# Kernel optimization log

Measured on AMD Instinct MI355X. Metric: run time of the kernel, lower is better.

The kernel has to match this reference:

```python
import jax, jax.numpy as jnp
import numpy as np

NUM_HEADS = 8
HEAD_DIM = 16


def setup_inputs() -> dict:
    key = jax.random.key(0)
    ks = jax.random.split(key, 9)
    B, S, E, H = 2, 4096, 16, 128
    sc_in = 1.0 / np.sqrt(E)
    sc_h = 1.0 / np.sqrt(H)
    return {
        "x": jax.random.normal(ks[0], (B, S, E), dtype=jnp.float32),
        "wq": jax.random.normal(ks[1], (H, E), dtype=jnp.float32) * sc_in,
        "bq": jax.random.normal(ks[2], (H,), dtype=jnp.float32) * 0.02,
        "wk": jax.random.normal(ks[3], (H, E), dtype=jnp.float32) * sc_in,
        "bk": jax.random.normal(ks[4], (H,), dtype=jnp.float32) * 0.02,
        "wv": jax.random.normal(ks[5], (H, E), dtype=jnp.float32) * sc_in,
        "bv": jax.random.normal(ks[6], (H,), dtype=jnp.float32) * 0.02,
        "wo": jax.random.normal(ks[7], (E, H), dtype=jnp.float32) * sc_h,
        "bo": jax.random.normal(ks[8], (E,), dtype=jnp.float32) * 0.02,
    }


def reference(x, wq, bq, wk, bk, wv, bv, wo, bo):
    B, S, E = x.shape
    H = wq.shape[0]
    nh, hd = NUM_HEADS, HEAD_DIM
    # QKV projections (torch Linear: y = x @ W.T + b)
    q = x @ wq.T + bq  # [B,S,H]
    k = x @ wk.T + bk
    v = x @ wv.T + bv
    # split heads -> [B,nh,S,hd]
    q = q.reshape(B, S, nh, hd).transpose(0, 2, 1, 3)
    k = k.reshape(B, S, nh, hd).transpose(0, 2, 1, 3)
    v = v.reshape(B, S, nh, hd).transpose(0, 2, 1, 3)
    # flex_attention with block_mask=None == full SDPA, scale = 1/sqrt(head_dim)
    scale = 1.0 / np.sqrt(hd)
    scores = jnp.einsum("bhqd,bhkd->bhqk", q, k) * scale  # [B,nh,S,S]
    attn = jax.nn.softmax(scores, axis=-1)
    out = jnp.einsum("bhqk,bhkd->bhqd", attn, v)  # [B,nh,S,hd]
    out = out.transpose(0, 2, 1, 3).reshape(B, S, H)
    return out @ wo.T + bo
```

## Files before the change

kernel.cpp:

```cpp
#include <hip/hip_runtime.h>
#include <hip/hip_bf16.h>
#include <math.h>

#define NH 8
#define HD 16
#define EE 16
#define HH 128
#define NCH 4
#define QR 32

typedef __attribute__((ext_vector_type(8)))  short short8;
typedef __attribute__((ext_vector_type(16))) float f32x16;
typedef __attribute__((ext_vector_type(4)))  float f32x4;

#define EXP2F(x) __builtin_amdgcn_exp2f(x)

__global__ __launch_bounds__(256) void qkv_fused(
        const float* __restrict__ x,
        const float* __restrict__ wq, const float* __restrict__ bq,
        const float* __restrict__ wk, const float* __restrict__ bk,
        const float* __restrict__ wv, const float* __restrict__ bv,
        __hip_bfloat16* __restrict__ Qb, __hip_bfloat16* __restrict__ Kb,
        __hip_bfloat16* __restrict__ Vt, int S) {
    int row0 = blockIdx.x * QR;
    int b = row0 / S, s0 = row0 - b * S;
    int tid = threadIdx.x;

    __shared__ __align__(16) float xs[QR][EE];
    __shared__ __align__(16) short qsb[QR][136];
    __shared__ __align__(16) short ksb[QR][136];
    __shared__ __align__(16) short vsb[QR][136];

    ((float*)xs)[tid]       = x[(size_t)row0 * EE + tid];
    ((float*)xs)[tid + 256] = x[(size_t)row0 * EE + tid + 256];
    __syncthreads();

    int h = tid & 127, sub = tid >> 7;
    float wqr[16], wkr[16], wvr[16];
    const float4* wq4 = (const float4*)(wq + h * EE);
    const float4* wk4 = (const float4*)(wk + h * EE);
    const float4* wv4 = (const float4*)(wv + h * EE);
#pragma unroll
    for (int j = 0; j < 4; ++j) {
        float4 a = wq4[j]; wqr[4*j]=a.x; wqr[4*j+1]=a.y; wqr[4*j+2]=a.z; wqr[4*j+3]=a.w;
        float4 c = wk4[j]; wkr[4*j]=c.x; wkr[4*j+1]=c.y; wkr[4*j+2]=c.z; wkr[4*j+3]=c.w;
        float4 d = wv4[j]; wvr[4*j]=d.x; wvr[4*j+1]=d.y; wvr[4*j+2]=d.z; wvr[4*j+3]=d.w;
    }
    float bqv = bq[h], bkv = bk[h], bvv = bv[h];

#pragma unroll
    for (int rr = 0; rr < 16; ++rr) {
        int r = (sub << 4) + rr;
        const float4* xv = (const float4*)xs[r];
        float aq = bqv, ak = bkv, av = bvv;
#pragma unroll
        for (int j = 0; j < 4; ++j) {
            float4 xe = xv[j];
            aq += xe.x*wqr[4*j] + xe.y*wqr[4*j+1] + xe.z*wqr[4*j+2] + xe.w*wqr[4*j+3];
            ak += xe.x*wkr[4*j] + xe.y*wkr[4*j+1] + xe.z*wkr[4*j+2] + xe.w*wkr[4*j+3];
            av += xe.x*wvr[4*j] + xe.y*wvr[4*j+1] + xe.z*wvr[4*j+2] + xe.w*wvr[4*j+3];
        }
        __hip_bfloat16 qb = __float2bfloat16(aq * 0.36067376022f);
        __hip_bfloat16 kb = __float2bfloat16(ak);
        __hip_bfloat16 vb = __float2bfloat16(av);
        qsb[r][h] = *reinterpret_cast<short*>(&qb);
        ksb[r][h] = *reinterpret_cast<short*>(&kb);
        vsb[r][h] = *reinterpret_cast<short*>(&vb);
    }
    __syncthreads();

    {
        int r = tid & 31, head = tid >> 5;
        short8 a = *(const short8*)&qsb[r][head * 16];
        short8 c = *(const short8*)&qsb[r][head * 16 + 8];
        short* dst = (short*)Qb + ((size_t)(b * NH + head) * S + s0 + r) * HD;
        *(short8*)dst = a;
        *(short8*)(dst + 8) = c;
        a = *(const short8*)&ksb[r][head * 16];
        c = *(const short8*)&ksb[r][head * 16 + 8];
        dst = (short*)Kb + ((size_t)(b * NH + head) * S + s0 + r) * HD;
        *(short8*)dst = a;
        *(short8*)(dst + 8) = c;
    }
    {
        int hd_idx = tid >> 1;
        int head2 = hd_idx >> 4, d2 = hd_idx & 15;
        int si0 = (tid & 1) * 16;
        short8 w0, w1;
#pragma unroll
        for (int j = 0; j < 8; ++j) w0[j] = vsb[si0 + j][hd_idx];
#pragma unroll
        for (int j = 0; j < 8; ++j) w1[j] = vsb[si0 + 8 + j][hd_idx];
        short* dst = (short*)Vt + ((size_t)(b * NH + head2) * HD + d2) * S + s0 + si0;
        *(short8*)dst = w0;
        *(short8*)(dst + 8) = w1;
    }
}

__global__ __launch_bounds__(256, 8) void attn(const __hip_bfloat16* __restrict__ Qb,
                                               const __hip_bfloat16* __restrict__ Kb,
                                               const __hip_bfloat16* __restrict__ Vtb,
                                               float* __restrict__ A,
                                               int S, int BH) {
    int bh = blockIdx.y;
    int q0 = blockIdx.x * 32;
    int cb = threadIdx.x >> 6;
    int lane = threadIdx.x & 63;
    int ql = lane & 31, half = lane >> 5;
    int l15 = lane & 15, l4 = lane >> 4;
    int CS = S / NCH;
    int kbeg = cb * CS;

    __shared__ __align__(16) union {
        short pt[NCH][32 * 40];
        struct { float o[NCH][32][16]; float l[NCH][32]; } red;
    } sm;
    short* pt = sm.pt[cb];

    const short* qptr = (const short*)Qb + ((size_t)bh * S + q0) * HD;
    const short* kf_ptr = (const short*)Kb + ((size_t)bh * S + kbeg + ql) * HD + 8 * half;
    const short* vf_ptr = (const short*)Vtb + ((size_t)bh * HD + l15) * S + kbeg + 8 * l4;

    short8 qf = *(const short8*)(qptr + ql * HD + 8 * half);

    f32x16 zc;
#pragma unroll
    for (int i = 0; i < 16; ++i) zc[i] = 0.f;

    float l = 0.f;
    f32x4 o0, o1;
#pragma unroll
    for (int i = 0; i < 4; ++i) { o0[i] = 0.f; o1[i] = 0.f; }

    for (int it = 0; it < CS / 32; ++it) {
        short8 kf = *(const short8*)kf_ptr;
        kf_ptr += 32 * HD;
        f32x16 st = __builtin_amdgcn_mfma_f32_32x32x16_bf16(kf, qf, zc, 0, 0, 0);

        float pf[16];
#pragma unroll
        for (int r = 0; r < 16; ++r) pf[r] = EXP2F(st[r]);
        float rs = ((pf[0] + pf[1]) + (pf[2] + pf[3])) + ((pf[4] + pf[5]) + (pf[6] + pf[7]))
                 + ((pf[8] + pf[9]) + (pf[10] + pf[11])) + ((pf[12] + pf[13]) + (pf[14] + pf[15]));
        l += rs;

        union PU { __hip_bfloat162 b2; unsigned u; };
        unsigned pk[8];
#pragma unroll
        for (int i = 0; i < 8; ++i) {
            float2 f2; f2.x = pf[2 * i]; f2.y = pf[2 * i + 1];
            PU pu; pu.b2 = __float22bfloat162_rn(f2);
            pk[i] = pu.u;
        }
#pragma unroll
        for (int i = 0; i < 4; ++i) {
            uint2 w; w.x = pk[2 * i]; w.y = pk[2 * i + 1];
            *(uint2*)&pt[ql * 40 + 8 * i + 4 * half] = w;
        }
        short8 p0 = *(const short8*)&pt[l15 * 40 + 8 * l4];
        short8 p1 = *(const short8*)&pt[(l15 + 16) * 40 + 8 * l4];
        short8 vf = *(const short8*)vf_ptr;
        vf_ptr += 32;

        o0 = __builtin_amdgcn_mfma_f32_16x16x32_bf16(vf, p0, o0, 0, 0, 0);
        o1 = __builtin_amdgcn_mfma_f32_16x16x32_bf16(vf, p1, o1, 0, 0, 0);
    }

    l += __shfl_xor(l, 32);

    __syncthreads();
    {
        float4 r0; r0.x = o0[0]; r0.y = o0[1]; r0.z = o0[2]; r0.w = o0[3];
        float4 r1; r1.x = o1[0]; r1.y = o1[1]; r1.z = o1[2]; r1.w = o1[3];
        *(float4*)&sm.red.o[cb][l15][4 * l4]      = r0;
        *(float4*)&sm.red.o[cb][l15 + 16][4 * l4] = r1;
        if (half == 0) sm.red.l[cb][ql] = l;
    }
    __syncthreads();

    if (threadIdx.x < 128) {
        int q = threadIdx.x >> 2, quad = threadIdx.x & 3;
        float4 acc; acc.x = 0.f; acc.y = 0.f; acc.z = 0.f; acc.w = 0.f;
        float ls = 0.f;
#pragma unroll
        for (int c = 0; c < NCH; ++c) {
            float4 v = *(const float4*)&sm.red.o[c][q][4 * quad];
            acc.x += v.x; acc.y += v.y; acc.z += v.z; acc.w += v.w;
            ls += sm.red.l[c][q];
        }
        float inv = 1.f / ls;
        acc.x *= inv; acc.y *= inv; acc.z *= inv; acc.w *= inv;
        int b = bh >> 3, head = bh & 7;
        *(float4*)&A[((size_t)(b * S + q0 + q)) * HH + head * HD + 4 * quad] = acc;
    }
}

__global__ __launch_bounds__(256) void out_proj(
        const float* __restrict__ A, const float* __restrict__ wo,
        const float* __restrict__ bo, float* __restrict__ out, int rows) {
    __shared__ float As[16][HH + 1];
    __shared__ float ws[EE][HH + 1];
    int r0 = blockIdx.x * 16;
    int tid = threadIdx.x;
#pragma unroll
    for (int i = 0; i < 8; ++i) {
        int idx = tid + i * 256;
        ws[idx >> 7][idx & 127] = wo[idx];
        As[idx >> 7][idx & 127] = A[(size_t)r0 * HH + idx];
    }
    __syncthreads();
    int r = tid >> 4, e = tid & 15;
    float acc = bo[e];
#pragma unroll
    for (int h = 0; h < HH; ++h) acc += As[r][h] * ws[e][h];
    out[(size_t)(r0 + r) * EE + e] = acc;
}

extern "C" void kernel_launch(void* const* d_in, const int* in_sizes, int n_in,
                              void* d_out, int out_size, void* d_ws, size_t ws_size,
                              hipStream_t stream) {
    const float* x  = (const float*)d_in[0];
    const float* wq = (const float*)d_in[1];
    const float* bq = (const float*)d_in[2];
    const float* wk = (const float*)d_in[3];
    const float* bk = (const float*)d_in[4];
    const float* wv = (const float*)d_in[5];
    const float* bv = (const float*)d_in[6];
    const float* wo = (const float*)d_in[7];
    const float* bo = (const float*)d_in[8];
    float* out = (float*)d_out;

    int rows = in_sizes[0] / EE;
    int S = 4096;
    int B = rows / S;
    int BH = B * NH;

    size_t n = (size_t)rows * HH;
    __hip_bfloat16* Qb = (__hip_bfloat16*)d_ws;
    __hip_bfloat16* Kb = Qb + n;
    __hip_bfloat16* Vt = Kb + n;
    float* A = (float*)(Vt + n);

    qkv_fused<<<rows / QR, 256, 0, stream>>>(x, wq, bq, wk, bk, wv, bv, Qb, Kb, Vt, S);
    dim3 g2(S / 32, BH);
    attn<<<g2, 256, 0, stream>>>(Qb, Kb, Vt, A, S, BH);
    out_proj<<<rows / 16, 256, 0, stream>>>(A, wo, bo, out, rows);
}
```

Before: 129.0 us.

## Fuse output projection into attention via per-head atomics; halve QKV tile rows

The output projection now runs in the attention kernel's epilogue. Each head block multiplies its normalized 32x16 output by its 16-column slice of wo, adds bo/NH, and atomically accumulates into the output, which is zeroed with a memset first. This removes the separate out_proj launch and the fp32 intermediate A's write and read. It costs a memset, 8-way atomic contention per output element and a non-deterministic summation order. Separately, the QKV kernel processes 16 rows per block instead of 32, which doubles the block count.

```diff
diff --git a/kernel.cpp b/kernel.cpp
--- a/kernel.cpp
+++ b/kernel.cpp
@@ -7,7 +7,7 @@
 #define EE 16
 #define HH 128
 #define NCH 4
-#define QR 32
+#define QR 16
 
 typedef __attribute__((ext_vector_type(8)))  short short8;
 typedef __attribute__((ext_vector_type(16))) float f32x16;
@@ -31,8 +31,7 @@
     __shared__ __align__(16) short ksb[QR][136];
     __shared__ __align__(16) short vsb[QR][136];
 
-    ((float*)xs)[tid]       = x[(size_t)row0 * EE + tid];
-    ((float*)xs)[tid + 256] = x[(size_t)row0 * EE + tid + 256];
+    ((float*)xs)[tid] = x[(size_t)row0 * EE + tid];
     __syncthreads();
 
     int h = tid & 127, sub = tid >> 7;
@@ -49,8 +48,8 @@
     float bqv = bq[h], bkv = bk[h], bvv = bv[h];
 
 #pragma unroll
-    for (int rr = 0; rr < 16; ++rr) {
-        int r = (sub << 4) + rr;
+    for (int rr = 0; rr < 8; ++rr) {
+        int r = (sub << 3) + rr;
         const float4* xv = (const float4*)xs[r];
         float aq = bqv, ak = bkv, av = bvv;
 #pragma unroll
@@ -70,37 +69,40 @@
     __syncthreads();
 
     {
-        int r = tid & 31, head = tid >> 5;
-        short8 a = *(const short8*)&qsb[r][head * 16];
-        short8 c = *(const short8*)&qsb[r][head * 16 + 8];
-        short* dst = (short*)Qb + ((size_t)(b * NH + head) * S + s0 + r) * HD;
-        *(short8*)dst = a;
-        *(short8*)(dst + 8) = c;
-        a = *(const short8*)&ksb[r][head * 16];
-        c = *(const short8*)&ksb[r][head * 16 + 8];
-        dst = (short*)Kb + ((size_t)(b * NH + head) * S + s0 + r) * HD;
-        *(short8*)dst = a;
-        *(short8*)(dst + 8) = c;
+        int pr = tid & 127;
+        int r = pr & 15, head = pr >> 4;
+        if (tid < 128) {
+            short8 a = *(const short8*)&qsb[r][head * 16];
+            short8 c = *(const short8*)&qsb[r][head * 16 + 8];
+            short* dst = (short*)Qb + ((size_t)(b * NH + head) * S + s0 + r) * HD;
+            *(short8*)dst = a;
+            *(short8*)(dst + 8) = c;
+        } else {
+            short8 a = *(const short8*)&ksb[r][head * 16];
+            short8 c = *(const short8*)&ksb[r][head * 16 + 8];
+            short* dst = (short*)Kb + ((size_t)(b * NH + head) * S + s0 + r) * HD;
+            *(short8*)dst = a;
+            *(short8*)(dst + 8) = c;
+        }
     }
     {
         int hd_idx = tid >> 1;
         int head2 = hd_idx >> 4, d2 = hd_idx & 15;
-        int si0 = (tid & 1) * 16;
-        short8 w0, w1;
+        int si0 = (tid & 1) * 8;
+        short8 w0;
 #pragma unroll
         for (int j = 0; j < 8; ++j) w0[j] = vsb[si0 + j][hd_idx];
-#pragma unroll
-        for (int j = 0; j < 8; ++j) w1[j] = vsb[si0 + 8 + j][hd_idx];
         short* dst = (short*)Vt + ((size_t)(b * NH + head2) * HD + d2) * S + s0 + si0;
         *(short8*)dst = w0;
-        *(short8*)(dst + 8) = w1;
     }
 }
 
 __global__ __launch_bounds__(256, 8) void attn(const __hip_bfloat16* __restrict__ Qb,
                                                const __hip_bfloat16* __restrict__ Kb,
                                                const __hip_bfloat16* __restrict__ Vtb,
-                                               float* __restrict__ A,
+                                               const float* __restrict__ wo,
+                                               const float* __restrict__ bo,
+                                               float* __restrict__ Out,
                                                int S, int BH) {
     int bh = blockIdx.y;
     int q0 = blockIdx.x * 32;
@@ -115,6 +117,7 @@
         short pt[NCH][32 * 40];
         struct { float o[NCH][32][16]; float l[NCH][32]; } red;
     } sm;
+    __shared__ __align__(16) float onorm[32][16];
     short* pt = sm.pt[cb];
 
     const short* qptr = (const short*)Qb + ((size_t)bh * S + q0) * HD;
@@ -190,30 +193,26 @@
         }
         float inv = 1.f / ls;
         acc.x *= inv; acc.y *= inv; acc.z *= inv; acc.w *= inv;
-        int b = bh >> 3, head = bh & 7;
-        *(float4*)&A[((size_t)(b * S + q0 + q)) * HH + head * HD + 4 * quad] = acc;
-    }
-}
-
-__global__ __launch_bounds__(256) void out_proj(
-        const float* __restrict__ A, const float* __restrict__ wo,
-        const float* __restrict__ bo, float* __restrict__ out, int rows) {
-    __shared__ float As[16][HH + 1];
-    __shared__ float ws[EE][HH + 1];
-    int r0 = blockIdx.x * 16;
-    int tid = threadIdx.x;
-#pragma unroll
-    for (int i = 0; i < 8; ++i) {
-        int idx = tid + i * 256;
-        ws[idx >> 7][idx & 127] = wo[idx];
-        As[idx >> 7][idx & 127] = A[(size_t)r0 * HH + idx];
-    }
-    __syncthreads();
-    int r = tid >> 4, e = tid & 15;
-    float acc = bo[e];
-#pragma unroll
-    for (int h = 0; h < HH; ++h) acc += As[r][h] * ws[e][h];
-    out[(size_t)(r0 + r) * EE + e] = acc;
+        *(float4*)&onorm[q][4 * quad] = acc;
+    }
+    __syncthreads();
+
+    int b = bh >> 3, head = bh & 7;
+#pragma unroll
+    for (int i = 0; i < 2; ++i) {
+        int p = threadIdx.x + 256 * i;
+        int q = p >> 4, e = p & 15;
+        const float4* w4 = (const float4*)(wo + e * HH + head * HD);
+        const float4* o4 = (const float4*)&onorm[q][0];
+        float acc = bo[e] * (1.0f / NH);
+#pragma unroll
+        for (int j = 0; j < 4; ++j) {
+            float4 w = w4[j];
+            float4 o = o4[j];
+            acc += w.x * o.x + w.y * o.y + w.z * o.z + w.w * o.w;
+        }
+        atomicAdd(&Out[((size_t)(b * S + q0 + q)) * EE + e], acc);
+    }
 }
 
 extern "C" void kernel_launch(void* const* d_in, const int* in_sizes, int n_in,
@@ -239,10 +238,9 @@
     __hip_bfloat16* Qb = (__hip_bfloat16*)d_ws;
     __hip_bfloat16* Kb = Qb + n;
     __hip_bfloat16* Vt = Kb + n;
-    float* A = (float*)(Vt + n);
-
+
+    hipMemsetAsync(out, 0, (size_t)out_size * sizeof(float), stream);
     qkv_fused<<<rows / QR, 256, 0, stream>>>(x, wq, bq, wk, bk, wv, bv, Qb, Kb, Vt, S);
     dim3 g2(S / 32, BH);
-    attn<<<g2, 256, 0, stream>>>(Qb, Kb, Vt, A, S, BH);
-    out_proj<<<rows / 16, 256, 0, stream>>>(A, wo, bo, out, rows);
+    attn<<<g2, 256, 0, stream>>>(Qb, Kb, Vt, wo, bo, out, S, BH);
 }
```

After: 129.1 us. No clear change (+0.0%).
